# Performance work log

Measured on AMD Instinct MI355X. Metric: run time of the kernel, lower is better.

Reference implementation:

```python
import jax, jax.numpy as jnp
import numpy as np

# dims
T, B, C_IN, C_OUT, NE, RD = 256, 8, 256, 256, 64, 64
TAU = 1.0          # gumbel_tau
COMMIT = 0.25      # commitment_scale
KMEANS = 1.0       # train_embeddings_scale
IMP = 30.0         # imp_loss_scale (hard-coded in module)


def setup_inputs() -> dict:
    key = jax.random.key(0)
    k0, k1, k2, k3 = jax.random.split(key, 4)
    a = np.sqrt(6.0) / (C_IN + C_OUT)  # dynamic_init_method==1 uniform bound
    return {
        "x": jax.random.normal(k0, (T, B, C_IN), jnp.float32),
        "map_w": jax.random.normal(k1, (RD, C_IN), jnp.float32) / np.sqrt(C_IN),
        "map_b": jnp.zeros((RD,), jnp.float32),
        "centroids": jax.random.normal(k2, (NE, RD), jnp.float32) * 0.5,
        "pw_w": jax.random.uniform(k3, (NE, C_OUT * C_IN), jnp.float32, -a, a),
        "pw_B": jnp.zeros((1, 1, C_OUT), jnp.float32),
    }


def reference(x, map_w, map_b, centroids, pw_w, pw_B):
    # key projection: (T*B, RD)
    k = x.reshape(T * B, C_IN) @ map_w.T + map_b
    # squared euclidean distances to centroids: (T*B, NE)
    d = (jnp.sum(k * k, axis=1, keepdims=True)
         + jnp.sum(centroids * centroids, axis=1)
         - 2.0 * (k @ centroids.T))
    # gumbel-softmax (soft, training path) with fixed noise
    g = jax.random.gumbel(jax.random.key(42), d.shape, d.dtype)
    resp = jax.nn.softmax((-d + g) / TAU, axis=-1)  # (T*B, NE)
    quantized = resp @ centroids                    # (T*B, RD)
    commitment_loss = jnp.mean((k - jax.lax.stop_gradient(quantized)) ** 2)
    kmeans_loss = jnp.mean((jax.lax.stop_gradient(k) - quantized) ** 2)
    importance = resp.sum(axis=0)                   # (NE,)
    imp_loss = jnp.std(importance, ddof=1) / jnp.mean(importance)
    loss = COMMIT * commitment_loss + IMP * imp_loss + KMEANS * kmeans_loss
    # soft expert-weight combine then per-token matvec
    w = (resp @ pw_w).reshape(T, B, C_OUT, C_IN)    # (T,B,out,in)
    out = jnp.einsum('tboi,tbi->tbo', w, x) + pw_B  # constant-bias mode
    return out, loss
```

## Files before the change

### kernel.cpp

```cpp
#include <hip/hip_runtime.h>
#include <stdint.h>

#define CIN   256
#define COUT  256
#define NE    64
#define RD    64
#define NTOK  2048

typedef __attribute__((ext_vector_type(8))) short bf16x8;
typedef __attribute__((ext_vector_type(4))) float f32x4;

__device__ inline unsigned short f2bf(float f) {
    uint32_t u = __float_as_uint(f);
    uint32_t r = (u + 0x7FFFu + ((u >> 16) & 1u)) >> 16;
    return (unsigned short)r;
}

__device__ inline float wave_sum(float v) {
    #pragma unroll
    for (int m = 1; m < 64; m <<= 1) v += __shfl_xor(v, m, 64);
    return v;
}
__device__ inline float wave_max(float v) {
    #pragma unroll
    for (int m = 1; m < 64; m <<= 1) v = fmaxf(v, __shfl_xor(v, m, 64));
    return v;
}

__device__ inline uint32_t rotl32(uint32_t v, int d) { return (v << d) | (v >> (32 - d)); }

__device__ inline void threefry_0_42(uint32_t c0, uint32_t c1, uint32_t& o0, uint32_t& o1) {
    const uint32_t ks0 = 0u, ks1 = 42u, ks2 = 0u ^ 42u ^ 0x1BD11BDAu;
    uint32_t x0 = c0 + ks0, x1 = c1 + ks1;
#define TF_R(r) { x0 += x1; x1 = rotl32(x1, r); x1 ^= x0; }
    TF_R(13) TF_R(15) TF_R(26) TF_R(6)
    x0 += ks1; x1 += ks2 + 1u;
    TF_R(17) TF_R(29) TF_R(16) TF_R(24)
    x0 += ks2; x1 += ks0 + 2u;
    TF_R(13) TF_R(15) TF_R(26) TF_R(6)
    x0 += ks0; x1 += ks1 + 3u;
    TF_R(17) TF_R(29) TF_R(16) TF_R(24)
    x0 += ks1; x1 += ks2 + 4u;
    TF_R(13) TF_R(15) TF_R(26) TF_R(6)
    x0 += ks2; x1 += ks0 + 5u;
#undef TF_R
    o0 = x0; o1 = x1;
}

__global__ __launch_bounds__(256) void vq_pack_kernel(
    const float* __restrict__ pw, unsigned short* __restrict__ Bp,
    const float* __restrict__ x, const float* __restrict__ mw,
    const float* __restrict__ mb, const float* __restrict__ cent,
    float* __restrict__ resp_out, float* __restrict__ commit_out)
{
    __shared__ float xs[4][CIN];
    __shared__ float cs[NE][RD + 1];
    __shared__ float ksh[4][RD];
    __shared__ float rs[4][NE];

    const int tid = threadIdx.x;

    if (blockIdx.x >= 512) {
        int G = (blockIdx.x - 512) * 256 + tid;
        int tile = G >> 8, qg = G & 255;
        int ct = tile >> 9, g = (tile >> 6) & 7, p = tile & 63;
        int e = (g << 3) + (p >> 3), kc = p & 7;
        int n = qg >> 2, gp = qg & 3;
        int k16 = gp ^ ((n >> 1) & 3);
        int o = (ct << 6) + n;
        const float* s = pw + ((size_t)e << 16) + (o << 8) + (kc << 5) + (k16 << 3);
        float4 v0 = *(const float4*)s;
        float4 v1 = *(const float4*)(s + 4);
        ushort4 a, b;
        a.x = f2bf(v0.x); a.y = f2bf(v0.y); a.z = f2bf(v0.z); a.w = f2bf(v0.w);
        b.x = f2bf(v1.x); b.y = f2bf(v1.y); b.z = f2bf(v1.z); b.w = f2bf(v1.w);
        *(ushort4*)(Bp + ((size_t)G << 3)) = a;
        *(ushort4*)(Bp + ((size_t)G << 3) + 4) = b;
        return;
    }

    const int w  = tid >> 6;
    const int t  = tid & 63;
    const int tb = (blockIdx.x << 2) + w;

    ((float4*)xs[w])[t] = ((const float4*)(x + (size_t)tb * CIN))[t];
    #pragma unroll
    for (int j = 0; j < 4; ++j) {
        int fidx = (j << 8) + tid;
        float4 v = ((const float4*)cent)[fidx];
        int row = fidx >> 4, c0 = (fidx & 15) << 2;
        cs[row][c0] = v.x; cs[row][c0 + 1] = v.y; cs[row][c0 + 2] = v.z; cs[row][c0 + 3] = v.w;
    }
    __syncthreads();

    float kr = mb[t];
    const float4* mwr = (const float4*)(mw + (size_t)t * CIN);
    #pragma unroll 8
    for (int j = 0; j < 64; ++j) {
        float4 wv = mwr[j];
        kr += wv.x * xs[w][(j << 2)] + wv.y * xs[w][(j << 2) + 1]
            + wv.z * xs[w][(j << 2) + 2] + wv.w * xs[w][(j << 2) + 3];
    }
    ksh[w][t] = kr;
    float kk = wave_sum(kr * kr);
    __syncthreads();

    float cc = 0.f, dt = 0.f;
    #pragma unroll 8
    for (int r = 0; r < 64; ++r) {
        float cv = cs[t][r];
        cc += cv * cv;
        dt += ksh[w][r] * cv;
    }
    float d = kk + cc - 2.f * dt;

    uint32_t fidx = (uint32_t)((tb << 6) + t);
    uint32_t cnt  = fidx < 65536u ? fidx : fidx - 65536u;
    uint32_t o0, o1;
    threefry_0_42(cnt, cnt + 65536u, o0, o1);
    uint32_t bits = fidx < 65536u ? o0 : o1;
    float uf = __uint_as_float((bits >> 9) | 0x3f800000u) - 1.0f;
    uf = fmaxf(uf, 1.17549435e-38f);
    float g2 = -logf(-logf(uf));

    float sv = g2 - d;
    float mx = wave_max(sv);
    float pz = expf(sv - mx);
    float ps = wave_sum(pz);
    float rv = pz / ps;
    resp_out[(tb << 6) + t] = rv;
    rs[w][t] = rv;
    __syncthreads();

    float q = 0.f;
    #pragma unroll 8
    for (int e2 = 0; e2 < 64; ++e2) q += rs[w][e2] * cs[e2][t];
    float df = kr - q;
    float sq = wave_sum(df * df);
    if (t == 0) commit_out[tb] = sq;
}

struct GemmRegs {
    f32x4 P0, P1, P2, P3;
    f32x4 O0, O1, O2, O3;
};

template<int T>
__device__ __attribute__((always_inline)) inline void stage16(
    const char* bsrc, char* Bb, int w, int lane)
{
    const char* src = bsrc + ((size_t)T << 14) + (w << 11) + (lane << 4);
    char* dst = Bb + ((T & 1) << 14) + (w << 11);
    __builtin_amdgcn_global_load_lds(
        (const __attribute__((address_space(1))) unsigned int*)src,
        (__attribute__((address_space(3))) unsigned int*)dst, 16, 0, 0);
    __builtin_amdgcn_global_load_lds(
        (const __attribute__((address_space(1))) unsigned int*)(src + 1024),
        (__attribute__((address_space(3))) unsigned int*)(dst + 1024), 16, 0, 0);
}

template<int T>
__device__ __attribute__((always_inline)) inline void phase(
    const char* bsrc, char* Bb,
    const bf16x8& a0, const bf16x8& a1, const bf16x8& a2, const bf16x8& a3,
    GemmRegs& R, const float (*rsh)[8], int w, int lane, int lo, int kq)
{
    if constexpr (T + 1 < 16) stage16<T + 1>(bsrc, Bb, w, lane);

    const char* bt = Bb + ((T & 1) << 14);
    #pragma unroll
    for (int kc = 0; kc < 4; ++kc) {
        const char* bk = bt + (kc << 12);
        bf16x8 b0, b1, b2, b3;
        { int n = lo;      b0 = *(const bf16x8*)(bk + (n << 6) + ((kq ^ ((n >> 1) & 3)) << 4)); }
        { int n = 16 + lo; b1 = *(const bf16x8*)(bk + (n << 6) + ((kq ^ ((n >> 1) & 3)) << 4)); }
        { int n = 32 + lo; b2 = *(const bf16x8*)(bk + (n << 6) + ((kq ^ ((n >> 1) & 3)) << 4)); }
        { int n = 48 + lo; b3 = *(const bf16x8*)(bk + (n << 6) + ((kq ^ ((n >> 1) & 3)) << 4)); }
        const bf16x8& a = (kc == 0) ? a0 : (kc == 1) ? a1 : (kc == 2) ? a2 : a3;
        R.P0 = __builtin_amdgcn_mfma_f32_16x16x32_bf16(a, b0, R.P0, 0, 0, 0);
        R.P1 = __builtin_amdgcn_mfma_f32_16x16x32_bf16(a, b1, R.P1, 0, 0, 0);
        R.P2 = __builtin_amdgcn_mfma_f32_16x16x32_bf16(a, b2, R.P2, 0, 0, 0);
        R.P3 = __builtin_amdgcn_mfma_f32_16x16x32_bf16(a, b3, R.P3, 0, 0, 0);
    }

    if constexpr (T & 1) {
        constexpr int el = T >> 1;
        const int rb = (w << 4) + (kq << 2);
        float r0 = rsh[rb + 0][el], r1 = rsh[rb + 1][el];
        float r2 = rsh[rb + 2][el], r3 = rsh[rb + 3][el];
        const f32x4 z = {};
        R.O0[0] += r0 * R.P0[0]; R.O0[1] += r1 * R.P0[1]; R.O0[2] += r2 * R.P0[2]; R.O0[3] += r3 * R.P0[3];
        R.O1[0] += r0 * R.P1[0]; R.O1[1] += r1 * R.P1[1]; R.O1[2] += r2 * R.P1[2]; R.O1[3] += r3 * R.P1[3];
        R.O2[0] += r0 * R.P2[0]; R.O2[1] += r1 * R.P2[1]; R.O2[2] += r2 * R.P2[2]; R.O2[3] += r3 * R.P2[3];
        R.O3[0] += r0 * R.P3[0]; R.O3[1] += r1 * R.P3[1]; R.O3[2] += r2 * R.P3[2]; R.O3[3] += r3 * R.P3[3];
        R.P0 = z; R.P1 = z; R.P2 = z; R.P3 = z;
    }
    __syncthreads();
}

#define LOAD_AF(name, idx) { \
    const float* s_ = xb + ((idx) << 5); \
    float4 v0_ = *(const float4*)s_; \
    float4 v1_ = *(const float4*)(s_ + 4); \
    bf16x8 bv_; \
    bv_[0] = (short)f2bf(v0_.x); bv_[1] = (short)f2bf(v0_.y); \
    bv_[2] = (short)f2bf(v0_.z); bv_[3] = (short)f2bf(v0_.w); \
    bv_[4] = (short)f2bf(v1_.x); bv_[5] = (short)f2bf(v1_.y); \
    bv_[6] = (short)f2bf(v1_.z); bv_[7] = (short)f2bf(v1_.w); \
    name = bv_; }

__global__ __launch_bounds__(512, 4) void gemm_kernel(
    const float* __restrict__ x, const float* __restrict__ resp,
    const unsigned short* __restrict__ Bp, float* __restrict__ partial)
{
    __shared__ char Bb[32768];
    __shared__ float rsh[128][8];

    const int tid  = threadIdx.x;
    const int lane = tid & 63;
    const int w    = tid >> 6;
    const int lo   = lane & 15, kq = lane >> 4;
    const int bid  = blockIdx.x;
    const int g    = bid & 7, ct = (bid >> 3) & 3, mt = bid >> 5;
    const int m0   = mt << 7;

    {
        int row = tid >> 2, e0 = (tid & 3) << 1;
        float2 rv = *(const float2*)(resp + ((size_t)(m0 + row) << 6) + (g << 3) + e0);
        *(float2*)(&rsh[row][e0]) = rv;
    }

    bf16x8 af0, af1, af2, af3, af4, af5, af6, af7;
    {
        const float* xb = x + ((size_t)(m0 + (w << 4) + lo) << 8) + (kq << 3);
        LOAD_AF(af0, 0) LOAD_AF(af1, 1) LOAD_AF(af2, 2) LOAD_AF(af3, 3)
        LOAD_AF(af4, 4) LOAD_AF(af5, 5) LOAD_AF(af6, 6) LOAD_AF(af7, 7)
    }

    const char* bsrc = (const char*)Bp + ((size_t)((ct << 3) + g) << 18);

    stage16<0>(bsrc, Bb, w, lane);
    __syncthreads();

    GemmRegs R = {};

    phase< 0>(bsrc, Bb, af0, af1, af2, af3, R, rsh, w, lane, lo, kq);
    phase< 1>(bsrc, Bb, af4, af5, af6, af7, R, rsh, w, lane, lo, kq);
    phase< 2>(bsrc, Bb, af0, af1, af2, af3, R, rsh, w, lane, lo, kq);
    phase< 3>(bsrc, Bb, af4, af5, af6, af7, R, rsh, w, lane, lo, kq);
    phase< 4>(bsrc, Bb, af0, af1, af2, af3, R, rsh, w, lane, lo, kq);
    phase< 5>(bsrc, Bb, af4, af5, af6, af7, R, rsh, w, lane, lo, kq);
    phase< 6>(bsrc, Bb, af0, af1, af2, af3, R, rsh, w, lane, lo, kq);
    phase< 7>(bsrc, Bb, af4, af5, af6, af7, R, rsh, w, lane, lo, kq);
    phase< 8>(bsrc, Bb, af0, af1, af2, af3, R, rsh, w, lane, lo, kq);
    phase< 9>(bsrc, Bb, af4, af5, af6, af7, R, rsh, w, lane, lo, kq);
    phase<10>(bsrc, Bb, af0, af1, af2, af3, R, rsh, w, lane, lo, kq);
    phase<11>(bsrc, Bb, af4, af5, af6, af7, R, rsh, w, lane, lo, kq);
    phase<12>(bsrc, Bb, af0, af1, af2, af3, R, rsh, w, lane, lo, kq);
    phase<13>(bsrc, Bb, af4, af5, af6, af7, R, rsh, w, lane, lo, kq);
    phase<14>(bsrc, Bb, af0, af1, af2, af3, R, rsh, w, lane, lo, kq);
    phase<15>(bsrc, Bb, af4, af5, af6, af7, R, rsh, w, lane, lo, kq);

    float* pout = partial + ((size_t)g << 19)
                + ((size_t)(m0 + (w << 4) + (kq << 2)) << 8) + (ct << 6) + lo;
    {
        float* pr;
        pr = pout;                    pr[0] = R.O0[0]; pr[16] = R.O1[0]; pr[32] = R.O2[0]; pr[48] = R.O3[0];
        pr = pout + 256;              pr[0] = R.O0[1]; pr[16] = R.O1[1]; pr[32] = R.O2[1]; pr[48] = R.O3[1];
        pr = pout + 512;              pr[0] = R.O0[2]; pr[16] = R.O1[2]; pr[32] = R.O2[2]; pr[48] = R.O3[2];
        pr = pout + 768;              pr[0] = R.O0[3]; pr[16] = R.O1[3]; pr[32] = R.O2[3]; pr[48] = R.O3[3];
    }
}

__global__ __launch_bounds__(256) void reduce_loss_kernel(
    const float* __restrict__ partial, const float* __restrict__ bias,
    float* __restrict__ out, const float* __restrict__ resp,
    const float* __restrict__ commit_part, float* __restrict__ imp_p,
    float* __restrict__ cm_p)
{
    __shared__ float part[4][64];
    const int t = threadIdx.x;

    if (blockIdx.x < 512) {
        int idx = blockIdx.x * 256 + t;
        float4 s = ((const float4*)bias)[idx & 63];
        #pragma unroll
        for (int g = 0; g < 8; ++g) {
            float4 v = ((const float4*)partial)[((size_t)g << 17) + idx];
            s.x += v.x; s.y += v.y; s.z += v.z; s.w += v.w;
        }
        ((float4*)out)[idx] = s;
        return;
    }

    const int b = blockIdx.x - 512;
    const int e = t & 63, grp = t >> 6;
    float s = 0.f;
    #pragma unroll
    for (int j = 0; j < 16; ++j)
        s += resp[(size_t)((b << 6) + (grp << 4) + j) * 64 + e];
    part[grp][e] = s;
    __syncthreads();
    if (t < 64) {
        float v = part[0][t] + part[1][t] + part[2][t] + part[3][t];
        imp_p[(b << 6) + t] = v;
        float cm = commit_part[(b << 6) + t];
        cm = wave_sum(cm);
        if (t == 0) cm_p[b] = cm;
    }
}

__global__ __launch_bounds__(64) void loss_final_kernel(const float* __restrict__ imp_p,
                                                        const float* __restrict__ cm_p,
                                                        float* __restrict__ loss_out)
{
    const int t = threadIdx.x;
    float imp = 0.f;
    #pragma unroll
    for (int b = 0; b < 32; ++b) imp += imp_p[(b << 6) + t];
    float ct = (t < 32) ? cm_p[t] : 0.f;
    ct = wave_sum(ct);
    float tot  = wave_sum(imp);
    float mean = tot * (1.0f / 64.f);
    float dv   = imp - mean;
    float var  = wave_sum(dv * dv) * (1.0f / 63.f);
    if (t == 0) {
        float mse = ct * (1.0f / (float)(NTOK * RD));
        float imp_loss = sqrtf(var) / mean;
        loss_out[0] = (0.25f + 1.0f) * mse + 30.0f * imp_loss;
    }
}

extern "C" void kernel_launch(void* const* d_in, const int* in_sizes, int n_in,
                              void* d_out, int out_size, void* d_ws, size_t ws_size,
                              hipStream_t stream)
{
    const float* x     = (const float*)d_in[0];
    const float* map_w = (const float*)d_in[1];
    const float* map_b = (const float*)d_in[2];
    const float* cent  = (const float*)d_in[3];
    const float* pw_w  = (const float*)d_in[4];
    const float* pw_B  = (const float*)d_in[5];
    float* out = (float*)d_out;

    char* ws = (char*)d_ws;
    float* resp        = (float*)ws;
    float* commit      = (float*)(ws + 524288);
    float* imp_p       = (float*)(ws + 540672);
    float* cm_p        = (float*)(ws + 557056);
    unsigned short* Bp = (unsigned short*)(ws + (1u << 20));
    float* partial     = (float*)(ws + (10u << 20));

    vq_pack_kernel<<<2560, 256, 0, stream>>>(pw_w, Bp, x, map_w, map_b, cent, resp, commit);
    gemm_kernel<<<512, 512, 0, stream>>>(x, resp, Bp, partial);
    reduce_loss_kernel<<<544, 256, 0, stream>>>(partial, pw_B, out, resp, commit, imp_p, cm_p);
    loss_final_kernel<<<1, 64, 0, stream>>>(imp_p, cm_p, out + NTOK * COUT);
}
```

Before: 57.61 us.

## Halve GEMM waves with 2x M-tile per wave and 4-stage LDS pipeline

The GEMM block drops from 8 to 4 waves, and each wave now computes two 16-row M subtiles, so every B fragment read from LDS feeds twice as many MFMAs. B staging becomes a quad-buffered ring in 64 KB of LDS, prefetched three stages ahead, with explicit vmcnt waits and raw s_barrier instead of a syncthreads per phase. The aim is to cut LDS read traffic per MFMA and hide global-to-LDS latency better. The cost is more registers per wave, fewer resident waves, and hand-tuned waitcnt logic that could race if the counts are wrong.

```diff
diff --git a/kernel.cpp b/kernel.cpp
--- a/kernel.cpp
+++ b/kernel.cpp
@@ -141,33 +141,38 @@
 }
 
 struct GemmRegs {
-    f32x4 P0, P1, P2, P3;
-    f32x4 O0, O1, O2, O3;
+    f32x4 P00, P01, P02, P03, P10, P11, P12, P13;
+    f32x4 O00, O01, O02, O03, O10, O11, O12, O13;
 };
 
 template<int T>
 __device__ __attribute__((always_inline)) inline void stage16(
     const char* bsrc, char* Bb, int w, int lane)
 {
-    const char* src = bsrc + ((size_t)T << 14) + (w << 11) + (lane << 4);
-    char* dst = Bb + ((T & 1) << 14) + (w << 11);
-    __builtin_amdgcn_global_load_lds(
-        (const __attribute__((address_space(1))) unsigned int*)src,
-        (__attribute__((address_space(3))) unsigned int*)dst, 16, 0, 0);
-    __builtin_amdgcn_global_load_lds(
-        (const __attribute__((address_space(1))) unsigned int*)(src + 1024),
-        (__attribute__((address_space(3))) unsigned int*)(dst + 1024), 16, 0, 0);
+    const char* src = bsrc + ((size_t)T << 14) + (w << 12) + (lane << 4);
+    char* dst = Bb + ((T & 3) << 14) + (w << 12);
+    #pragma unroll
+    for (int i = 0; i < 4; ++i)
+        __builtin_amdgcn_global_load_lds(
+            (const __attribute__((address_space(1))) unsigned int*)(src + (i << 10)),
+            (__attribute__((address_space(3))) unsigned int*)(dst + (i << 10)), 16, 0, 0);
 }
 
 template<int T>
 __device__ __attribute__((always_inline)) inline void phase(
     const char* bsrc, char* Bb,
-    const bf16x8& a0, const bf16x8& a1, const bf16x8& a2, const bf16x8& a3,
+    const bf16x8& a00, const bf16x8& a01, const bf16x8& a02, const bf16x8& a03,
+    const bf16x8& a10, const bf16x8& a11, const bf16x8& a12, const bf16x8& a13,
     GemmRegs& R, const float (*rsh)[8], int w, int lane, int lo, int kq)
 {
-    if constexpr (T + 1 < 16) stage16<T + 1>(bsrc, Bb, w, lane);
-
-    const char* bt = Bb + ((T & 1) << 14);
+    if constexpr (T <= 13)      asm volatile("s_waitcnt vmcnt(8)" ::: "memory");
+    else if constexpr (T == 14) asm volatile("s_waitcnt vmcnt(4)" ::: "memory");
+    else                        asm volatile("s_waitcnt vmcnt(0)" ::: "memory");
+    asm volatile("s_barrier" ::: "memory");
+
+    if constexpr (T + 3 < 16) stage16<T + 3>(bsrc, Bb, w, lane);
+
+    const char* bt = Bb + ((T & 3) << 14);
     #pragma unroll
     for (int kc = 0; kc < 4; ++kc) {
         const char* bk = bt + (kc << 12);
@@ -176,30 +181,41 @@
         { int n = 16 + lo; b1 = *(const bf16x8*)(bk + (n << 6) + ((kq ^ ((n >> 1) & 3)) << 4)); }
         { int n = 32 + lo; b2 = *(const bf16x8*)(bk + (n << 6) + ((kq ^ ((n >> 1) & 3)) << 4)); }
         { int n = 48 + lo; b3 = *(const bf16x8*)(bk + (n << 6) + ((kq ^ ((n >> 1) & 3)) << 4)); }
-        const bf16x8& a = (kc == 0) ? a0 : (kc == 1) ? a1 : (kc == 2) ? a2 : a3;
-        R.P0 = __builtin_amdgcn_mfma_f32_16x16x32_bf16(a, b0, R.P0, 0, 0, 0);
-        R.P1 = __builtin_amdgcn_mfma_f32_16x16x32_bf16(a, b1, R.P1, 0, 0, 0);
-        R.P2 = __builtin_amdgcn_mfma_f32_16x16x32_bf16(a, b2, R.P2, 0, 0, 0);
-        R.P3 = __builtin_amdgcn_mfma_f32_16x16x32_bf16(a, b3, R.P3, 0, 0, 0);
+        const bf16x8& am0 = (kc == 0) ? a00 : (kc == 1) ? a01 : (kc == 2) ? a02 : a03;
+        const bf16x8& am1 = (kc == 0) ? a10 : (kc == 1) ? a11 : (kc == 2) ? a12 : a13;
+        R.P00 = __builtin_amdgcn_mfma_f32_16x16x32_bf16(am0, b0, R.P00, 0, 0, 0);
+        R.P01 = __builtin_amdgcn_mfma_f32_16x16x32_bf16(am0, b1, R.P01, 0, 0, 0);
+        R.P02 = __builtin_amdgcn_mfma_f32_16x16x32_bf16(am0, b2, R.P02, 0, 0, 0);
+        R.P03 = __builtin_amdgcn_mfma_f32_16x16x32_bf16(am0, b3, R.P03, 0, 0, 0);
+        R.P10 = __builtin_amdgcn_mfma_f32_16x16x32_bf16(am1, b0, R.P10, 0, 0, 0);
+        R.P11 = __builtin_amdgcn_mfma_f32_16x16x32_bf16(am1, b1, R.P11, 0, 0, 0);
+        R.P12 = __builtin_amdgcn_mfma_f32_16x16x32_bf16(am1, b2, R.P12, 0, 0, 0);
+        R.P13 = __builtin_amdgcn_mfma_f32_16x16x32_bf16(am1, b3, R.P13, 0, 0, 0);
     }
 
     if constexpr (T & 1) {
         constexpr int el = T >> 1;
-        const int rb = (w << 4) + (kq << 2);
-        float r0 = rsh[rb + 0][el], r1 = rsh[rb + 1][el];
-        float r2 = rsh[rb + 2][el], r3 = rsh[rb + 3][el];
+        const int rb = (w << 5) + (kq << 2);
+        float r00 = rsh[rb +  0][el], r01 = rsh[rb +  1][el];
+        float r02 = rsh[rb +  2][el], r03 = rsh[rb +  3][el];
+        float r10 = rsh[rb + 16][el], r11 = rsh[rb + 17][el];
+        float r12 = rsh[rb + 18][el], r13 = rsh[rb + 19][el];
         const f32x4 z = {};
-        R.O0[0] += r0 * R.P0[0]; R.O0[1] += r1 * R.P0[1]; R.O0[2] += r2 * R.P0[2]; R.O0[3] += r3 * R.P0[3];
-        R.O1[0] += r0 * R.P1[0]; R.O1[1] += r1 * R.P1[1]; R.O1[2] += r2 * R.P1[2]; R.O1[3] += r3 * R.P1[3];
-        R.O2[0] += r0 * R.P2[0]; R.O2[1] += r1 * R.P2[1]; R.O2[2] += r2 * R.P2[2]; R.O2[3] += r3 * R.P2[3];
-        R.O3[0] += r0 * R.P3[0]; R.O3[1] += r1 * R.P3[1]; R.O3[2] += r2 * R.P3[2]; R.O3[3] += r3 * R.P3[3];
-        R.P0 = z; R.P1 = z; R.P2 = z; R.P3 = z;
-    }
-    __syncthreads();
-}
-
-#define LOAD_AF(name, idx) { \
-    const float* s_ = xb + ((idx) << 5); \
+        R.O00[0] += r00 * R.P00[0]; R.O00[1] += r01 * R.P00[1]; R.O00[2] += r02 * R.P00[2]; R.O00[3] += r03 * R.P00[3];
+        R.O01[0] += r00 * R.P01[0]; R.O01[1] += r01 * R.P01[1]; R.O01[2] += r02 * R.P01[2]; R.O01[3] += r03 * R.P01[3];
+        R.O02[0] += r00 * R.P02[0]; R.O02[1] += r01 * R.P02[1]; R.O02[2] += r02 * R.P02[2]; R.O02[3] += r03 * R.P02[3];
+        R.O03[0] += r00 * R.P03[0]; R.O03[1] += r01 * R.P03[1]; R.O03[2] += r02 * R.P03[2]; R.O03[3] += r03 * R.P03[3];
+        R.O10[0] += r10 * R.P10[0]; R.O10[1] += r11 * R.P10[1]; R.O10[2] += r12 * R.P10[2]; R.O10[3] += r13 * R.P10[3];
+        R.O11[0] += r10 * R.P11[0]; R.O11[1] += r11 * R.P11[1]; R.O11[2] += r12 * R.P11[2]; R.O11[3] += r13 * R.P11[3];
+        R.O12[0] += r10 * R.P12[0]; R.O12[1] += r11 * R.P12[1]; R.O12[2] += r12 * R.P12[2]; R.O12[3] += r13 * R.P12[3];
+        R.O13[0] += r10 * R.P13[0]; R.O13[1] += r11 * R.P13[1]; R.O13[2] += r12 * R.P13[2]; R.O13[3] += r13 * R.P13[3];
+        R.P00 = z; R.P01 = z; R.P02 = z; R.P03 = z;
+        R.P10 = z; R.P11 = z; R.P12 = z; R.P13 = z;
+    }
+}
+
+#define LOAD_AF(name, base, idx) { \
+    const float* s_ = (base) + ((idx) << 5); \
     float4 v0_ = *(const float4*)s_; \
     float4 v1_ = *(const float4*)(s_ + 4); \
     bf16x8 bv_; \
@@ -209,11 +225,11 @@
     bv_[6] = (short)f2bf(v1_.z); bv_[7] = (short)f2bf(v1_.w); \
     name = bv_; }
 
-__global__ __launch_bounds__(512, 4) void gemm_kernel(
+__global__ __launch_bounds__(256, 2) void gemm_kernel(
     const float* __restrict__ x, const float* __restrict__ resp,
     const unsigned short* __restrict__ Bp, float* __restrict__ partial)
 {
-    __shared__ char Bb[32768];
+    __shared__ char Bb[65536];
     __shared__ float rsh[128][8];
 
     const int tid  = threadIdx.x;
@@ -225,50 +241,63 @@
     const int m0   = mt << 7;
 
     {
-        int row = tid >> 2, e0 = (tid & 3) << 1;
-        float2 rv = *(const float2*)(resp + ((size_t)(m0 + row) << 6) + (g << 3) + e0);
-        *(float2*)(&rsh[row][e0]) = rv;
-    }
-
-    bf16x8 af0, af1, af2, af3, af4, af5, af6, af7;
+        int idx = tid << 2;
+        int row = idx >> 3, e0 = idx & 7;
+        float4 rv = *(const float4*)(resp + ((size_t)(m0 + row) << 6) + (g << 3) + e0);
+        *(float4*)(&rsh[row][e0]) = rv;
+    }
+
+    bf16x8 af00, af01, af02, af03, af04, af05, af06, af07;
+    bf16x8 af10, af11, af12, af13, af14, af15, af16, af17;
     {
-        const float* xb = x + ((size_t)(m0 + (w << 4) + lo) << 8) + (kq << 3);
-        LOAD_AF(af0, 0) LOAD_AF(af1, 1) LOAD_AF(af2, 2) LOAD_AF(af3, 3)
-        LOAD_AF(af4, 4) LOAD_AF(af5, 5) LOAD_AF(af6, 6) LOAD_AF(af7, 7)
+        const float* xb0 = x + ((size_t)(m0 + (w << 5) + lo) << 8) + (kq << 3);
+        const float* xb1 = xb0 + (16 << 8);
+        LOAD_AF(af00, xb0, 0) LOAD_AF(af01, xb0, 1) LOAD_AF(af02, xb0, 2) LOAD_AF(af03, xb0, 3)
+        LOAD_AF(af04, xb0, 4) LOAD_AF(af05, xb0, 5) LOAD_AF(af06, xb0, 6) LOAD_AF(af07, xb0, 7)
+        LOAD_AF(af10, xb1, 0) LOAD_AF(af11, xb1, 1) LOAD_AF(af12, xb1, 2) LOAD_AF(af13, xb1, 3)
+        LOAD_AF(af14, xb1, 4) LOAD_AF(af15, xb1, 5) LOAD_AF(af16, xb1, 6) LOAD_AF(af17, xb1, 7)
     }
 
     const char* bsrc = (const char*)Bp + ((size_t)((ct << 3) + g) << 18);
 
+    asm volatile("s_waitcnt vmcnt(0)" ::: "memory");
+    asm volatile("s_waitcnt lgkmcnt(0)" ::: "memory");
+
     stage16<0>(bsrc, Bb, w, lane);
-    __syncthreads();
+    stage16<1>(bsrc, Bb, w, lane);
+    stage16<2>(bsrc, Bb, w, lane);
 
     GemmRegs R = {};
 
-    phase< 0>(bsrc, Bb, af0, af1, af2, af3, R, rsh, w, lane, lo, kq);
-    phase< 1>(bsrc, Bb, af4, af5, af6, af7, R, rsh, w, lane, lo, kq);
-    phase< 2>(bsrc, Bb, af0, af1, af2, af3, R, rsh, w, lane, lo, kq);
-    phase< 3>(bsrc, Bb, af4, af5, af6, af7, R, rsh, w, lane, lo, kq);
-    phase< 4>(bsrc, Bb, af0, af1, af2, af3, R, rsh, w, lane, lo, kq);
-    phase< 5>(bsrc, Bb, af4, af5, af6, af7, R, rsh, w, lane, lo, kq);
-    phase< 6>(bsrc, Bb, af0, af1, af2, af3, R, rsh, w, lane, lo, kq);
-    phase< 7>(bsrc, Bb, af4, af5, af6, af7, R, rsh, w, lane, lo, kq);
-    phase< 8>(bsrc, Bb, af0, af1, af2, af3, R, rsh, w, lane, lo, kq);
-    phase< 9>(bsrc, Bb, af4, af5, af6, af7, R, rsh, w, lane, lo, kq);
-    phase<10>(bsrc, Bb, af0, af1, af2, af3, R, rsh, w, lane, lo, kq);
-    phase<11>(bsrc, Bb, af4, af5, af6, af7, R, rsh, w, lane, lo, kq);
-    phase<12>(bsrc, Bb, af0, af1, af2, af3, R, rsh, w, lane, lo, kq);
-    phase<13>(bsrc, Bb, af4, af5, af6, af7, R, rsh, w, lane, lo, kq);
-    phase<14>(bsrc, Bb, af0, af1, af2, af3, R, rsh, w, lane, lo, kq);
-    phase<15>(bsrc, Bb, af4, af5, af6, af7, R, rsh, w, lane, lo, kq);
+    phase< 0>(bsrc, Bb, af00, af01, af02, af03, af10, af11, af12, af13, R, rsh, w, lane, lo, kq);
+    phase< 1>(bsrc, Bb, af04, af05, af06, af07, af14, af15, af16, af17, R, rsh, w, lane, lo, kq);
+    phase< 2>(bsrc, Bb, af00, af01, af02, af03, af10, af11, af12, af13, R, rsh, w, lane, lo, kq);
+    phase< 3>(bsrc, Bb, af04, af05, af06, af07, af14, af15, af16, af17, R, rsh, w, lane, lo, kq);
+    phase< 4>(bsrc, Bb, af00, af01, af02, af03, af10, af11, af12, af13, R, rsh, w, lane, lo, kq);
+    phase< 5>(bsrc, Bb, af04, af05, af06, af07, af14, af15, af16, af17, R, rsh, w, lane, lo, kq);
+    phase< 6>(bsrc, Bb, af00, af01, af02, af03, af10, af11, af12, af13, R, rsh, w, lane, lo, kq);
+    phase< 7>(bsrc, Bb, af04, af05, af06, af07, af14, af15, af16, af17, R, rsh, w, lane, lo, kq);
+    phase< 8>(bsrc, Bb, af00, af01, af02, af03, af10, af11, af12, af13, R, rsh, w, lane, lo, kq);
+    phase< 9>(bsrc, Bb, af04, af05, af06, af07, af14, af15, af16, af17, R, rsh, w, lane, lo, kq);
+    phase<10>(bsrc, Bb, af00, af01, af02, af03, af10, af11, af12, af13, R, rsh, w, lane, lo, kq);
+    phase<11>(bsrc, Bb, af04, af05, af06, af07, af14, af15, af16, af17, R, rsh, w, lane, lo, kq);
+    phase<12>(bsrc, Bb, af00, af01, af02, af03, af10, af11, af12, af13, R, rsh, w, lane, lo, kq);
+    phase<13>(bsrc, Bb, af04, af05, af06, af07, af14, af15, af16, af17, R, rsh, w, lane, lo, kq);
+    phase<14>(bsrc, Bb, af00, af01, af02, af03, af10, af11, af12, af13, R, rsh, w, lane, lo, kq);
+    phase<15>(bsrc, Bb, af04, af05, af06, af07, af14, af15, af16, af17, R, rsh, w, lane, lo, kq);
 
     float* pout = partial + ((size_t)g << 19)
-                + ((size_t)(m0 + (w << 4) + (kq << 2)) << 8) + (ct << 6) + lo;
+                + ((size_t)(m0 + (w << 5) + (kq << 2)) << 8) + (ct << 6) + lo;
     {
         float* pr;
-        pr = pout;                    pr[0] = R.O0[0]; pr[16] = R.O1[0]; pr[32] = R.O2[0]; pr[48] = R.O3[0];
-        pr = pout + 256;              pr[0] = R.O0[1]; pr[16] = R.O1[1]; pr[32] = R.O2[1]; pr[48] = R.O3[1];
-        pr = pout + 512;              pr[0] = R.O0[2]; pr[16] = R.O1[2]; pr[32] = R.O2[2]; pr[48] = R.O3[2];
-        pr = pout + 768;              pr[0] = R.O0[3]; pr[16] = R.O1[3]; pr[32] = R.O2[3]; pr[48] = R.O3[3];
+        pr = pout;                  pr[0] = R.O00[0]; pr[16] = R.O01[0]; pr[32] = R.O02[0]; pr[48] = R.O03[0];
+        pr = pout + 256;            pr[0] = R.O00[1]; pr[16] = R.O01[1]; pr[32] = R.O02[1]; pr[48] = R.O03[1];
+        pr = pout + 512;            pr[0] = R.O00[2]; pr[16] = R.O01[2]; pr[32] = R.O02[2]; pr[48] = R.O03[2];
+        pr = pout + 768;            pr[0] = R.O00[3]; pr[16] = R.O01[3]; pr[32] = R.O02[3]; pr[48] = R.O03[3];
+        pr = pout + 4096;           pr[0] = R.O10[0]; pr[16] = R.O11[0]; pr[32] = R.O12[0]; pr[48] = R.O13[0];
+        pr = pout + 4096 + 256;     pr[0] = R.O10[1]; pr[16] = R.O11[1]; pr[32] = R.O12[1]; pr[48] = R.O13[1];
+        pr = pout + 4096 + 512;     pr[0] = R.O10[2]; pr[16] = R.O11[2]; pr[32] = R.O12[2]; pr[48] = R.O13[2];
+        pr = pout + 4096 + 768;     pr[0] = R.O10[3]; pr[16] = R.O11[3]; pr[32] = R.O12[3]; pr[48] = R.O13[3];
     }
 }
 
@@ -352,7 +381,7 @@
     float* partial     = (float*)(ws + (10u << 20));
 
     vq_pack_kernel<<<2560, 256, 0, stream>>>(pw_w, Bp, x, map_w, map_b, cent, resp, commit);
-    gemm_kernel<<<512, 512, 0, stream>>>(x, resp, Bp, partial);
+    gemm_kernel<<<512, 256, 0, stream>>>(x, resp, Bp, partial);
     reduce_loss_kernel<<<544, 256, 0, stream>>>(partial, pw_B, out, resp, commit, imp_p, cm_p);
     loss_final_kernel<<<1, 64, 0, stream>>>(imp_p, cm_p, out + NTOK * COUT);
 }
```

Result: no change. 57.07 us (-0.9%).

## Retile expert GEMM to 256-row blocks with 4-stage LDS pipeline

Applied to the files above, without the earlier changes.

The GEMM tile changes from 128 rows by 64 output columns to 256 rows by 32 columns with 4 waves of 256 threads. Each wave now owns 64 rows with 32 A fragments held in registers. B staging moves to a 4-slot ring of 4 KB chunks, three loads in flight, explicit vmcnt waits and raw s_barrier in place of __syncthreads. The pack kernel's B layout and swizzle are rewritten to match. The aim is more reuse of each B tile across rows and deeper load/compute overlap, at the cost of much higher register pressure and lower occupancy.

```diff
diff --git a/kernel.cpp b/kernel.cpp
--- a/kernel.cpp
+++ b/kernel.cpp
@@ -63,12 +63,13 @@
     if (blockIdx.x >= 512) {
         int G = (blockIdx.x - 512) * 256 + tid;
         int tile = G >> 8, qg = G & 255;
-        int ct = tile >> 9, g = (tile >> 6) & 7, p = tile & 63;
-        int e = (g << 3) + (p >> 3), kc = p & 7;
-        int n = qg >> 2, gp = qg & 3;
-        int k16 = gp ^ ((n >> 1) & 3);
-        int o = (ct << 6) + n;
-        const float* s = pw + ((size_t)e << 16) + (o << 8) + (kc << 5) + (k16 << 3);
+        int ct = tile >> 8, g = (tile >> 5) & 7, p = tile & 31;
+        int e = (g << 3) + (p >> 2);
+        int n = qg >> 3, gp = qg & 7;
+        int k16 = gp ^ (n & 7);
+        int o = (ct << 5) + n;
+        int i = ((p & 3) << 6) + (k16 << 3);
+        const float* s = pw + ((size_t)e << 16) + (o << 8) + i;
         float4 v0 = *(const float4*)s;
         float4 v1 = *(const float4*)(s + 4);
         ushort4 a, b;
@@ -141,135 +142,154 @@
 }
 
 struct GemmRegs {
-    f32x4 P0, P1, P2, P3;
-    f32x4 O0, O1, O2, O3;
+    f32x4 P00, P01, P10, P11, P20, P21, P30, P31;
+    f32x4 O00, O01, O10, O11, O20, O21, O30, O31;
 };
 
 template<int T>
-__device__ __attribute__((always_inline)) inline void stage16(
+__device__ __attribute__((always_inline)) inline void stage4(
     const char* bsrc, char* Bb, int w, int lane)
 {
-    const char* src = bsrc + ((size_t)T << 14) + (w << 11) + (lane << 4);
-    char* dst = Bb + ((T & 1) << 14) + (w << 11);
     __builtin_amdgcn_global_load_lds(
-        (const __attribute__((address_space(1))) unsigned int*)src,
-        (__attribute__((address_space(3))) unsigned int*)dst, 16, 0, 0);
-    __builtin_amdgcn_global_load_lds(
-        (const __attribute__((address_space(1))) unsigned int*)(src + 1024),
-        (__attribute__((address_space(3))) unsigned int*)(dst + 1024), 16, 0, 0);
+        (const __attribute__((address_space(1))) unsigned int*)
+            (bsrc + ((size_t)T << 12) + (w << 10) + (lane << 4)),
+        (__attribute__((address_space(3))) unsigned int*)
+            (Bb + ((T & 3) << 12) + (w << 10)), 16, 0, 0);
 }
 
 template<int T>
 __device__ __attribute__((always_inline)) inline void phase(
     const char* bsrc, char* Bb,
-    const bf16x8& a0, const bf16x8& a1, const bf16x8& a2, const bf16x8& a3,
+    const bf16x8& a00, const bf16x8& a10, const bf16x8& a20, const bf16x8& a30,
+    const bf16x8& a01, const bf16x8& a11, const bf16x8& a21, const bf16x8& a31,
     GemmRegs& R, const float (*rsh)[8], int w, int lane, int lo, int kq)
 {
-    if constexpr (T + 1 < 16) stage16<T + 1>(bsrc, Bb, w, lane);
-
-    const char* bt = Bb + ((T & 1) << 14);
-    #pragma unroll
-    for (int kc = 0; kc < 4; ++kc) {
-        const char* bk = bt + (kc << 12);
-        bf16x8 b0, b1, b2, b3;
-        { int n = lo;      b0 = *(const bf16x8*)(bk + (n << 6) + ((kq ^ ((n >> 1) & 3)) << 4)); }
-        { int n = 16 + lo; b1 = *(const bf16x8*)(bk + (n << 6) + ((kq ^ ((n >> 1) & 3)) << 4)); }
-        { int n = 32 + lo; b2 = *(const bf16x8*)(bk + (n << 6) + ((kq ^ ((n >> 1) & 3)) << 4)); }
-        { int n = 48 + lo; b3 = *(const bf16x8*)(bk + (n << 6) + ((kq ^ ((n >> 1) & 3)) << 4)); }
-        const bf16x8& a = (kc == 0) ? a0 : (kc == 1) ? a1 : (kc == 2) ? a2 : a3;
-        R.P0 = __builtin_amdgcn_mfma_f32_16x16x32_bf16(a, b0, R.P0, 0, 0, 0);
-        R.P1 = __builtin_amdgcn_mfma_f32_16x16x32_bf16(a, b1, R.P1, 0, 0, 0);
-        R.P2 = __builtin_amdgcn_mfma_f32_16x16x32_bf16(a, b2, R.P2, 0, 0, 0);
-        R.P3 = __builtin_amdgcn_mfma_f32_16x16x32_bf16(a, b3, R.P3, 0, 0, 0);
-    }
-
-    if constexpr (T & 1) {
-        constexpr int el = T >> 1;
-        const int rb = (w << 4) + (kq << 2);
-        float r0 = rsh[rb + 0][el], r1 = rsh[rb + 1][el];
-        float r2 = rsh[rb + 2][el], r3 = rsh[rb + 3][el];
+    if constexpr (T <= 29)      asm volatile("s_waitcnt vmcnt(2)" ::: "memory");
+    else if constexpr (T == 30) asm volatile("s_waitcnt vmcnt(1)" ::: "memory");
+    else                        asm volatile("s_waitcnt vmcnt(0)" ::: "memory");
+    asm volatile("s_barrier" ::: "memory");
+
+    if constexpr (T + 3 < 32) stage4<T + 3>(bsrc, Bb, w, lane);
+
+    const char* bt = Bb + ((T & 3) << 12);
+    bf16x8 b00, b10, b01, b11;
+    { int n = lo;      b00 = *(const bf16x8*)(bt + (n << 7) + (((kq)     ^ (n & 7)) << 4)); }
+    { int n = 16 + lo; b10 = *(const bf16x8*)(bt + (n << 7) + (((kq)     ^ (n & 7)) << 4)); }
+    { int n = lo;      b01 = *(const bf16x8*)(bt + (n << 7) + (((4 + kq) ^ (n & 7)) << 4)); }
+    { int n = 16 + lo; b11 = *(const bf16x8*)(bt + (n << 7) + (((4 + kq) ^ (n & 7)) << 4)); }
+
+    R.P00 = __builtin_amdgcn_mfma_f32_16x16x32_bf16(a00, b00, R.P00, 0, 0, 0);
+    R.P01 = __builtin_amdgcn_mfma_f32_16x16x32_bf16(a00, b10, R.P01, 0, 0, 0);
+    R.P10 = __builtin_amdgcn_mfma_f32_16x16x32_bf16(a10, b00, R.P10, 0, 0, 0);
+    R.P11 = __builtin_amdgcn_mfma_f32_16x16x32_bf16(a10, b10, R.P11, 0, 0, 0);
+    R.P20 = __builtin_amdgcn_mfma_f32_16x16x32_bf16(a20, b00, R.P20, 0, 0, 0);
+    R.P21 = __builtin_amdgcn_mfma_f32_16x16x32_bf16(a20, b10, R.P21, 0, 0, 0);
+    R.P30 = __builtin_amdgcn_mfma_f32_16x16x32_bf16(a30, b00, R.P30, 0, 0, 0);
+    R.P31 = __builtin_amdgcn_mfma_f32_16x16x32_bf16(a30, b10, R.P31, 0, 0, 0);
+    R.P00 = __builtin_amdgcn_mfma_f32_16x16x32_bf16(a01, b01, R.P00, 0, 0, 0);
+    R.P01 = __builtin_amdgcn_mfma_f32_16x16x32_bf16(a01, b11, R.P01, 0, 0, 0);
+    R.P10 = __builtin_amdgcn_mfma_f32_16x16x32_bf16(a11, b01, R.P10, 0, 0, 0);
+    R.P11 = __builtin_amdgcn_mfma_f32_16x16x32_bf16(a11, b11, R.P11, 0, 0, 0);
+    R.P20 = __builtin_amdgcn_mfma_f32_16x16x32_bf16(a21, b01, R.P20, 0, 0, 0);
+    R.P21 = __builtin_amdgcn_mfma_f32_16x16x32_bf16(a21, b11, R.P21, 0, 0, 0);
+    R.P30 = __builtin_amdgcn_mfma_f32_16x16x32_bf16(a31, b01, R.P30, 0, 0, 0);
+    R.P31 = __builtin_amdgcn_mfma_f32_16x16x32_bf16(a31, b11, R.P31, 0, 0, 0);
+
+    if constexpr ((T & 3) == 3) {
+        constexpr int el = T >> 2;
+        const int rb = (w << 6) + (kq << 2);
         const f32x4 z = {};
-        R.O0[0] += r0 * R.P0[0]; R.O0[1] += r1 * R.P0[1]; R.O0[2] += r2 * R.P0[2]; R.O0[3] += r3 * R.P0[3];
-        R.O1[0] += r0 * R.P1[0]; R.O1[1] += r1 * R.P1[1]; R.O1[2] += r2 * R.P1[2]; R.O1[3] += r3 * R.P1[3];
-        R.O2[0] += r0 * R.P2[0]; R.O2[1] += r1 * R.P2[1]; R.O2[2] += r2 * R.P2[2]; R.O2[3] += r3 * R.P2[3];
-        R.O3[0] += r0 * R.P3[0]; R.O3[1] += r1 * R.P3[1]; R.O3[2] += r2 * R.P3[2]; R.O3[3] += r3 * R.P3[3];
-        R.P0 = z; R.P1 = z; R.P2 = z; R.P3 = z;
-    }
-    __syncthreads();
-}
-
-#define LOAD_AF(name, idx) { \
-    const float* s_ = xb + ((idx) << 5); \
-    float4 v0_ = *(const float4*)s_; \
-    float4 v1_ = *(const float4*)(s_ + 4); \
-    bf16x8 bv_; \
-    bv_[0] = (short)f2bf(v0_.x); bv_[1] = (short)f2bf(v0_.y); \
-    bv_[2] = (short)f2bf(v0_.z); bv_[3] = (short)f2bf(v0_.w); \
-    bv_[4] = (short)f2bf(v1_.x); bv_[5] = (short)f2bf(v1_.y); \
-    bv_[6] = (short)f2bf(v1_.z); bv_[7] = (short)f2bf(v1_.w); \
-    name = bv_; }
-
-__global__ __launch_bounds__(512, 4) void gemm_kernel(
+#define EPI(MI) { \
+        float r0_ = rsh[rb + (MI << 4) + 0][el], r1_ = rsh[rb + (MI << 4) + 1][el]; \
+        float r2_ = rsh[rb + (MI << 4) + 2][el], r3_ = rsh[rb + (MI << 4) + 3][el]; \
+        R.O##MI##0[0] += r0_ * R.P##MI##0[0]; R.O##MI##0[1] += r1_ * R.P##MI##0[1]; \
+        R.O##MI##0[2] += r2_ * R.P##MI##0[2]; R.O##MI##0[3] += r3_ * R.P##MI##0[3]; \
+        R.O##MI##1[0] += r0_ * R.P##MI##1[0]; R.O##MI##1[1] += r1_ * R.P##MI##1[1]; \
+        R.O##MI##1[2] += r2_ * R.P##MI##1[2]; R.O##MI##1[3] += r3_ * R.P##MI##1[3]; \
+        R.P##MI##0 = z; R.P##MI##1 = z; }
+        EPI(0) EPI(1) EPI(2) EPI(3)
+#undef EPI
+    }
+}
+
+__global__ __launch_bounds__(256, 2) void gemm_kernel(
     const float* __restrict__ x, const float* __restrict__ resp,
     const unsigned short* __restrict__ Bp, float* __restrict__ partial)
 {
-    __shared__ char Bb[32768];
-    __shared__ float rsh[128][8];
+    __shared__ char Bb[16384];
+    __shared__ float rsh[256][8];
 
     const int tid  = threadIdx.x;
     const int lane = tid & 63;
     const int w    = tid >> 6;
     const int lo   = lane & 15, kq = lane >> 4;
     const int bid  = blockIdx.x;
-    const int g    = bid & 7, ct = (bid >> 3) & 3, mt = bid >> 5;
-    const int m0   = mt << 7;
+    const int g    = bid & 7, ct = (bid >> 3) & 7, mt = bid >> 6;
+    const int m0   = mt << 8;
 
     {
-        int row = tid >> 2, e0 = (tid & 3) << 1;
-        float2 rv = *(const float2*)(resp + ((size_t)(m0 + row) << 6) + (g << 3) + e0);
-        *(float2*)(&rsh[row][e0]) = rv;
-    }
-
-    bf16x8 af0, af1, af2, af3, af4, af5, af6, af7;
+        float4 r0 = *(const float4*)(resp + ((size_t)(m0 + tid) << 6) + (g << 3));
+        float4 r1 = *(const float4*)(resp + ((size_t)(m0 + tid) << 6) + (g << 3) + 4);
+        *(float4*)(&rsh[tid][0]) = r0;
+        *(float4*)(&rsh[tid][4]) = r1;
+    }
+
+    bf16x8 af00, af01, af02, af03, af04, af05, af06, af07;
+    bf16x8 af10, af11, af12, af13, af14, af15, af16, af17;
+    bf16x8 af20, af21, af22, af23, af24, af25, af26, af27;
+    bf16x8 af30, af31, af32, af33, af34, af35, af36, af37;
     {
-        const float* xb = x + ((size_t)(m0 + (w << 4) + lo) << 8) + (kq << 3);
-        LOAD_AF(af0, 0) LOAD_AF(af1, 1) LOAD_AF(af2, 2) LOAD_AF(af3, 3)
-        LOAD_AF(af4, 4) LOAD_AF(af5, 5) LOAD_AF(af6, 6) LOAD_AF(af7, 7)
-    }
-
-    const char* bsrc = (const char*)Bp + ((size_t)((ct << 3) + g) << 18);
-
-    stage16<0>(bsrc, Bb, w, lane);
-    __syncthreads();
+        const float* xb = x + ((size_t)(m0 + (w << 6) + lo) << 8) + (kq << 3);
+#define LAF(MI, KC) { \
+        const float* s_ = xb + (MI * 4096) + (KC * 32); \
+        float4 v0_ = *(const float4*)s_; \
+        float4 v1_ = *(const float4*)(s_ + 4); \
+        bf16x8 bv_; \
+        bv_[0] = (short)f2bf(v0_.x); bv_[1] = (short)f2bf(v0_.y); \
+        bv_[2] = (short)f2bf(v0_.z); bv_[3] = (short)f2bf(v0_.w); \
+        bv_[4] = (short)f2bf(v1_.x); bv_[5] = (short)f2bf(v1_.y); \
+        bv_[6] = (short)f2bf(v1_.z); bv_[7] = (short)f2bf(v1_.w); \
+        af##MI##KC = bv_; }
+        LAF(0,0) LAF(0,1) LAF(0,2) LAF(0,3) LAF(0,4) LAF(0,5) LAF(0,6) LAF(0,7)
+        LAF(1,0) LAF(1,1) LAF(1,2) LAF(1,3) LAF(1,4) LAF(1,5) LAF(1,6) LAF(1,7)
+        LAF(2,0) LAF(2,1) LAF(2,2) LAF(2,3) LAF(2,4) LAF(2,5) LAF(2,6) LAF(2,7)
+        LAF(3,0) LAF(3,1) LAF(3,2) LAF(3,3) LAF(3,4) LAF(3,5) LAF(3,6) LAF(3,7)
+#undef LAF
+    }
+
+    const char* bsrc = (const char*)Bp + ((size_t)((ct << 3) + g) << 17);
+
+    asm volatile("s_waitcnt vmcnt(0)" ::: "memory");
+    asm volatile("s_waitcnt lgkmcnt(0)" ::: "memory");
+
+    stage4<0>(bsrc, Bb, w, lane);
+    stage4<1>(bsrc, Bb, w, lane);
+    stage4<2>(bsrc, Bb, w, lane);
 
     GemmRegs R = {};
 
-    phase< 0>(bsrc, Bb, af0, af1, af2, af3, R, rsh, w, lane, lo, kq);
-    phase< 1>(bsrc, Bb, af4, af5, af6, af7, R, rsh, w, lane, lo, kq);
-    phase< 2>(bsrc, Bb, af0, af1, af2, af3, R, rsh, w, lane, lo, kq);
-    phase< 3>(bsrc, Bb, af4, af5, af6, af7, R, rsh, w, lane, lo, kq);
-    phase< 4>(bsrc, Bb, af0, af1, af2, af3, R, rsh, w, lane, lo, kq);
-    phase< 5>(bsrc, Bb, af4, af5, af6, af7, R, rsh, w, lane, lo, kq);
-    phase< 6>(bsrc, Bb, af0, af1, af2, af3, R, rsh, w, lane, lo, kq);
-    phase< 7>(bsrc, Bb, af4, af5, af6, af7, R, rsh, w, lane, lo, kq);
-    phase< 8>(bsrc, Bb, af0, af1, af2, af3, R, rsh, w, lane, lo, kq);
-    phase< 9>(bsrc, Bb, af4, af5, af6, af7, R, rsh, w, lane, lo, kq);
-    phase<10>(bsrc, Bb, af0, af1, af2, af3, R, rsh, w, lane, lo, kq);
-    phase<11>(bsrc, Bb, af4, af5, af6, af7, R, rsh, w, lane, lo, kq);
-    phase<12>(bsrc, Bb, af0, af1, af2, af3, R, rsh, w, lane, lo, kq);
-    phase<13>(bsrc, Bb, af4, af5, af6, af7, R, rsh, w, lane, lo, kq);
-    phase<14>(bsrc, Bb, af0, af1, af2, af3, R, rsh, w, lane, lo, kq);
-    phase<15>(bsrc, Bb, af4, af5, af6, af7, R, rsh, w, lane, lo, kq);
+#define CPH(T, KA, KB) phase<T>(bsrc, Bb, \
+        af0##KA, af1##KA, af2##KA, af3##KA, \
+        af0##KB, af1##KB, af2##KB, af3##KB, R, rsh, w, lane, lo, kq);
+    CPH( 0,0,1) CPH( 1,2,3) CPH( 2,4,5) CPH( 3,6,7)
+    CPH( 4,0,1) CPH( 5,2,3) CPH( 6,4,5) CPH( 7,6,7)
+    CPH( 8,0,1) CPH( 9,2,3) CPH(10,4,5) CPH(11,6,7)
+    CPH(12,0,1) CPH(13,2,3) CPH(14,4,5) CPH(15,6,7)
+    CPH(16,0,1) CPH(17,2,3) CPH(18,4,5) CPH(19,6,7)
+    CPH(20,0,1) CPH(21,2,3) CPH(22,4,5) CPH(23,6,7)
+    CPH(24,0,1) CPH(25,2,3) CPH(26,4,5) CPH(27,6,7)
+    CPH(28,0,1) CPH(29,2,3) CPH(30,4,5) CPH(31,6,7)
+#undef CPH
 
     float* pout = partial + ((size_t)g << 19)
-                + ((size_t)(m0 + (w << 4) + (kq << 2)) << 8) + (ct << 6) + lo;
-    {
-        float* pr;
-        pr = pout;                    pr[0] = R.O0[0]; pr[16] = R.O1[0]; pr[32] = R.O2[0]; pr[48] = R.O3[0];
-        pr = pout + 256;              pr[0] = R.O0[1]; pr[16] = R.O1[1]; pr[32] = R.O2[1]; pr[48] = R.O3[1];
-        pr = pout + 512;              pr[0] = R.O0[2]; pr[16] = R.O1[2]; pr[32] = R.O2[2]; pr[48] = R.O3[2];
-        pr = pout + 768;              pr[0] = R.O0[3]; pr[16] = R.O1[3]; pr[32] = R.O2[3]; pr[48] = R.O3[3];
-    }
+                + ((size_t)(m0 + (w << 6) + (kq << 2)) << 8) + (ct << 5) + lo;
+#define STO(MI) { \
+        float* p0_ = pout + (((MI << 4) + 0) << 8); p0_[0] = R.O##MI##0[0]; p0_[16] = R.O##MI##1[0]; \
+        float* p1_ = pout + (((MI << 4) + 1) << 8); p1_[0] = R.O##MI##0[1]; p1_[16] = R.O##MI##1[1]; \
+        float* p2_ = pout + (((MI << 4) + 2) << 8); p2_[0] = R.O##MI##0[2]; p2_[16] = R.O##MI##1[2]; \
+        float* p3_ = pout + (((MI << 4) + 3) << 8); p3_[0] = R.O##MI##0[3]; p3_[16] = R.O##MI##1[3]; }
+    STO(0) STO(1) STO(2) STO(3)
+#undef STO
 }
 
 __global__ __launch_bounds__(256) void reduce_loss_kernel(
@@ -352,7 +372,7 @@
     float* partial     = (float*)(ws + (10u << 20));
 
     vq_pack_kernel<<<2560, 256, 0, stream>>>(pw_w, Bp, x, map_w, map_b, cent, resp, commit);
-    gemm_kernel<<<512, 512, 0, stream>>>(x, resp, Bp, partial);
+    gemm_kernel<<<512, 256, 0, stream>>>(x, resp, Bp, partial);
     reduce_loss_kernel<<<544, 256, 0, stream>>>(partial, pw_B, out, resp, commit, imp_p, cm_p);
     loss_final_kernel<<<1, 64, 0, stream>>>(imp_p, cm_p, out + NTOK * COUT);
 }
```

Result: slower. 70.72 us (+22.8%).
